# Kernel optimization log

Hardware: AMD Instinct MI355X
Metric: run time of the kernel (lower is better)

The kernel has to match this reference:

```python
import jax, jax.numpy as jnp
import numpy as np
import math

D = 128    # d_model
H = 8      # n_heads
NK = 16    # n_know
BS = 4
S = 256
DK = D // H
NEG = -1e32
LN_EPS = 1e-5


def _linear(x, W, b):
    return x @ W.T + b


def _layernorm(x, g, b):
    m = x.mean(-1, keepdims=True)
    v = ((x - m) ** 2).mean(-1, keepdims=True)
    return (x - m) / jnp.sqrt(v + LN_EPS) * g + b


def _attention(q, k, v, mask, gamma, maxout):
    # q,k,v: (B, H, S, DK); mask: (1,1,S,S) bool; gamma: (H,1,1)
    d_k = q.shape[-1]
    scores = jnp.einsum('bhid,bhjd->bhij', q, k) / math.sqrt(d_k)
    seqlen = scores.shape[-1]
    x = jnp.arange(seqlen, dtype=jnp.float32)
    pos = jnp.abs(x[None, :] - x[:, None])  # |j - i|, (S, S)
    # --- time-decay block (computed under no_grad in torch) ---
    s_ = jax.nn.softmax(jnp.where(mask, scores, NEG), axis=-1)
    distcum = jnp.cumsum(s_, axis=-1)
    disttotal = jnp.sum(s_, axis=-1, keepdims=True)
    dist = jnp.sqrt(jnp.clip((disttotal - distcum) * pos[None, None], 0.0, None))
    dist = jax.lax.stop_gradient(dist)
    effect = jnp.clip(jnp.exp(dist * (-jnp.abs(gamma)[None])), 1e-5, 1e5)
    scores = scores * effect
    scores = jax.nn.softmax(jnp.where(mask, scores, NEG), axis=-1)
    scores = jnp.where(mask, scores, 0.0)
    if maxout:
        scale = jnp.minimum(1.0 / scores.max(axis=-1, keepdims=True), 5.0)
        scores = scores * scale
    out = jnp.einsum('bhij,bhjd->bhid', scores, v)
    return out, scores


def _mha(q, k, v, mask, Wq, bq, Wk, bk, Wv, bv, Wo, bo, gamma, maxout):
    bs, seqlen, d = q.shape
    split = lambda x: x.reshape(bs, seqlen, H, DK).transpose(0, 2, 1, 3)
    qh = split(_linear(q, Wq, bq))
    kh = split(_linear(k, Wk, bk))
    vh = split(_linear(v, Wv, bv))
    out, scores = _attention(qh, kh, vh, mask, gamma, maxout)
    concat = out.transpose(0, 2, 1, 3).reshape(bs, seqlen, d)
    return _linear(concat, Wo, bo), scores


def _layer(query, key, values, peek_cur, Wq, bq, Wk, bk, Wv, bv, Wo, bo, gamma, lng, lnb):
    seqlen = query.shape[1]
    mask = jnp.tril(jnp.ones((seqlen, seqlen), bool), 0 if peek_cur else -1)[None, None]
    out, scores = _mha(query, key, values, mask, Wq, bq, Wk, bk, Wv, bv, Wo, bo, gamma,
                       maxout=not peek_cur)
    return _layernorm(query + out, lng, lnb), scores


def setup_inputs() -> dict:
    key = jax.random.key(0)
    ks = jax.random.split(key, 24)
    rn = lambda k, shape: (jax.random.normal(k, shape, jnp.float32) / math.sqrt(D))
    inp = {
        'q_emb': jax.random.normal(ks[0], (BS, S, D), jnp.float32),
        's_emb': jax.random.normal(ks[1], (BS, S, D), jnp.float32),
        'lens': jax.random.randint(ks[2], (BS,), 5, S),
        # block1 (kq_same=True -> shares Wq for K)
        'b1_Wq': rn(ks[3], (D, D)), 'b1_bq': jnp.zeros((D,), jnp.float32),
        'b1_Wv': rn(ks[4], (D, D)), 'b1_bv': jnp.zeros((D,), jnp.float32),
        'b1_Wo': rn(ks[5], (D, D)), 'b1_bo': jnp.zeros((D,), jnp.float32),
        'b1_gamma': jax.random.uniform(ks[6], (H, 1, 1), jnp.float32, -1.0, 1.0),
        'b1_lng': jnp.ones((D,), jnp.float32), 'b1_lnb': jnp.zeros((D,), jnp.float32),
        # block4 (kq_same=False)
        'b4_Wq': rn(ks[7], (D, D)), 'b4_bq': jnp.zeros((D,), jnp.float32),
        'b4_Wk': rn(ks[8], (D, D)), 'b4_bk': jnp.zeros((D,), jnp.float32),
        'b4_Wv': rn(ks[9], (D, D)), 'b4_bv': jnp.zeros((D,), jnp.float32),
        'b4_Wo': rn(ks[10], (D, D)), 'b4_bo': jnp.zeros((D,), jnp.float32),
        'b4_gamma': jax.random.uniform(ks[11], (H, 1, 1), jnp.float32, -1.0, 1.0),
        'b4_lng': jnp.ones((D,), jnp.float32), 'b4_lnb': jnp.zeros((D,), jnp.float32),
        'know_params': jax.random.uniform(ks[12], (NK, D), jnp.float32, -1.0, 1.0),
    }
    return inp


def reference(q_emb, s_emb, lens,
              b1_Wq, b1_bq, b1_Wv, b1_bv, b1_Wo, b1_bo, b1_gamma, b1_lng, b1_lnb,
              b4_Wq, b4_bq, b4_Wk, b4_bk, b4_Wv, b4_bv, b4_Wo, b4_bo, b4_gamma, b4_lng, b4_lnb,
              know_params):
    # n_layers == 1 path, eval mode (no mask dropout); lens unused in eval math.
    hq = q_emb
    p, q_scores = _layer(q_emb, q_emb, s_emb, True,
                         b1_Wq, b1_bq, b1_Wq, b1_bq, b1_Wv, b1_bv, b1_Wo, b1_bo,
                         b1_gamma, b1_lng, b1_lnb)
    bs, seqlen, d = p.shape
    query = jnp.broadcast_to(know_params[None, :, None, :], (bs, NK, seqlen, d)).reshape(bs * NK, seqlen, d)
    hq_r = jnp.broadcast_to(hq[:, None], (bs, NK, seqlen, d)).reshape(bs * NK, seqlen, d)
    p_r = jnp.broadcast_to(p[:, None], (bs, NK, seqlen, d)).reshape(bs * NK, seqlen, d)
    z, k_scores = _layer(query, hq_r, p_r, False,
                         b4_Wq, b4_bq, b4_Wk, b4_bk, b4_Wv, b4_bv, b4_Wo, b4_bo,
                         b4_gamma, b4_lng, b4_lnb)
    z = z.reshape(bs, NK, seqlen, d).transpose(0, 2, 1, 3).reshape(bs, seqlen, NK * d)
    k_scores = k_scores.reshape(bs, NK, H, seqlen, seqlen).transpose(0, 2, 3, 1, 4)
    return z, q_scores, k_scores
```

## Files before the change

### kernel.cpp

```cpp
#include <hip/hip_runtime.h>
#include <hip/hip_bf16.h>

#define DEV __device__ __forceinline__

DEV float4 f4fma(float4 a, float s, float4 w){
  a.x = fmaf(s, w.x, a.x); a.y = fmaf(s, w.y, a.y);
  a.z = fmaf(s, w.z, a.z); a.w = fmaf(s, w.w, a.w);
  return a;
}
DEV float4 f4add(float4 a, float4 b){
  a.x+=b.x; a.y+=b.y; a.z+=b.z; a.w+=b.w; return a;
}

DEV float waveAllMax(float x){
  #pragma unroll
  for(int o=1;o<64;o<<=1) x = fmaxf(x, __shfl_xor(x,o,64));
  return x;
}
DEV float waveAllSum(float x){
  #pragma unroll
  for(int o=1;o<64;o<<=1) x += __shfl_xor(x,o,64);
  return x;
}
DEV float waveReduceMax(float x){
  #pragma unroll
  for(int o=32;o>0;o>>=1) x = fmaxf(x, __shfl_down(x,o,64));
  return x;
}
DEV float blockMax256(float x, float* sc){
  int lane = threadIdx.x & 63, wid = threadIdx.x >> 6;
  x = waveReduceMax(x);
  __syncthreads();
  if(lane==0) sc[wid] = x;
  __syncthreads();
  return fmaxf(fmaxf(sc[0],sc[1]), fmaxf(sc[2],sc[3]));
}
DEV float blockScan256(float x, float* sc, float& total){
  int lane = threadIdx.x & 63, wid = threadIdx.x >> 6;
  float v = x;
  #pragma unroll
  for(int o=1;o<64;o<<=1){ float t = __shfl_up(v,o,64); if(lane>=o) v += t; }
  __syncthreads();
  if(lane==63) sc[wid] = v;
  __syncthreads();
  float pre=0.f, tot=0.f;
  #pragma unroll
  for(int ww=0;ww<4;ww++){ float s = sc[ww]; tot += s; if(ww<wid) pre += s; }
  total = tot;
  return v + pre;
}

template<int EPI>
DEV void gemm16_body(const float* __restrict__ in, const float* __restrict__ W,
                     const float* __restrict__ bias, const float* __restrict__ aux,
                     const float* __restrict__ lng, const float* __restrict__ lnb,
                     float* __restrict__ out, int r0, int nrows,
                     float* sWT, float (*sIn)[128])
{
  const int t = threadIdx.x;
  for(int idx=t; idx<2048; idx+=256){
    int r = idx>>7, c = idx&127;
    int row = r0+r;
    sIn[r][c] = (row<nrows) ? in[(size_t)row*128+c] : 0.f;
  }
  const int og = t & 31, rg = t >> 5;
  const int o0 = og*4;
  const float* s0p = sIn[rg*2];
  const float* s1p = sIn[rg*2+1];
  float4 a0 = make_float4(0,0,0,0), a1 = make_float4(0,0,0,0);

  #pragma unroll
  for(int half=0; half<2; half++){
    int c0 = half*64;
    __syncthreads();
    for(int idx=t; idx<8192; idx+=256){
      int o = idx>>6, cc = idx&63;
      sWT[cc*132 + o] = W[o*128 + c0 + cc];
    }
    __syncthreads();
    #pragma unroll 4
    for(int c=0;c<64;c+=4){
      float4 sA = *(const float4*)(s0p + c0 + c);
      float4 sB = *(const float4*)(s1p + c0 + c);
      const float* wp = sWT + c*132 + o0;
      float4 w0 = *(const float4*)(wp);
      float4 w1 = *(const float4*)(wp + 132);
      float4 w2 = *(const float4*)(wp + 264);
      float4 w3 = *(const float4*)(wp + 396);
      a0 = f4fma(a0, sA.x, w0); a0 = f4fma(a0, sA.y, w1);
      a0 = f4fma(a0, sA.z, w2); a0 = f4fma(a0, sA.w, w3);
      a1 = f4fma(a1, sB.x, w0); a1 = f4fma(a1, sB.y, w1);
      a1 = f4fma(a1, sB.z, w2); a1 = f4fma(a1, sB.w, w3);
    }
  }
  float4 bv = *(const float4*)(bias + o0);
  a0 = f4add(a0, bv); a1 = f4add(a1, bv);
  int row0 = r0 + rg*2, row1 = row0 + 1;

  if(EPI == 0){
    if(row0 < nrows) *(float4*)(out + (size_t)row0*128 + o0) = a0;
    if(row1 < nrows) *(float4*)(out + (size_t)row1*128 + o0) = a1;
  } else {
    const float *x0, *x1;
    if(EPI == 1){
      x0 = aux + (size_t)row0*128; x1 = aux + (size_t)row1*128;
    } else {
      x0 = aux + ((row0>>8)&15)*128; x1 = aux + ((row1>>8)&15)*128;
    }
    a0 = f4add(a0, *(const float4*)(x0 + o0));
    a1 = f4add(a1, *(const float4*)(x1 + o0));
    float s0 = a0.x+a0.y+a0.z+a0.w, s1 = a1.x+a1.y+a1.z+a1.w;
    float q0 = a0.x*a0.x+a0.y*a0.y+a0.z*a0.z+a0.w*a0.w;
    float q1 = a1.x*a1.x+a1.y*a1.y+a1.z*a1.z+a1.w*a1.w;
    #pragma unroll
    for(int o=1;o<32;o<<=1){
      s0 += __shfl_xor(s0,o,64); q0 += __shfl_xor(q0,o,64);
      s1 += __shfl_xor(s1,o,64); q1 += __shfl_xor(q1,o,64);
    }
    float m0 = s0*0.0078125f, v0 = q0*0.0078125f - m0*m0;
    float m1 = s1*0.0078125f, v1 = q1*0.0078125f - m1*m1;
    float i0 = rsqrtf(v0+1e-5f), i1 = rsqrtf(v1+1e-5f);
    float4 g  = *(const float4*)(lng + o0);
    float4 b2 = *(const float4*)(lnb + o0);
    float4 y0, y1;
    y0.x=(a0.x-m0)*i0*g.x+b2.x; y0.y=(a0.y-m0)*i0*g.y+b2.y;
    y0.z=(a0.z-m0)*i0*g.z+b2.z; y0.w=(a0.w-m0)*i0*g.w+b2.w;
    y1.x=(a1.x-m1)*i1*g.x+b2.x; y1.y=(a1.y-m1)*i1*g.y+b2.y;
    y1.z=(a1.z-m1)*i1*g.z+b2.z; y1.w=(a1.w-m1)*i1*g.w+b2.w;
    float *p0, *p1;
    if(EPI == 1){
      p0 = out + (size_t)row0*128; p1 = out + (size_t)row1*128;
    } else {
      int n0=(row0>>8)&15, b0=row0>>12, i0i=row0&255;
      int n1=(row1>>8)&15, b1=row1>>12, i1i=row1&255;
      p0 = out + ((((size_t)b0*256+i0i)*16+n0)<<7);
      p1 = out + ((((size_t)b1*256+i1i)*16+n1)<<7);
    }
    *(float4*)(p0 + o0) = y0;
    *(float4*)(p1 + o0) = y1;
  }
}

template<int EPI>
__global__ __launch_bounds__(256) void gemm16_kernel(
  const float* __restrict__ in, const float* __restrict__ W,
  const float* __restrict__ bias, const float* __restrict__ aux,
  const float* __restrict__ lng, const float* __restrict__ lnb,
  float* __restrict__ out, int nrows)
{
  __shared__ float sWT[64*132];
  __shared__ float sIn[16][128];
  gemm16_body<EPI>(in, W, bias, aux, lng, lnb, out, blockIdx.x*16, nrows, sWT, sIn);
}

__global__ __launch_bounds__(256) void proj4_kernel(
  const float* __restrict__ in0, const float* __restrict__ W0, const float* __restrict__ b0, float* __restrict__ o0,
  const float* __restrict__ in1, const float* __restrict__ W1, const float* __restrict__ b1, float* __restrict__ o1,
  const float* __restrict__ in2, const float* __restrict__ W2, const float* __restrict__ b2, float* __restrict__ o2,
  const float* __restrict__ in3, const float* __restrict__ W3, const float* __restrict__ b3, float* __restrict__ o3)
{
  __shared__ float sWT[64*132];
  __shared__ float sIn[16][128];
  int bb = blockIdx.x;
  if(bb < 64)       gemm16_body<0>(in0,W0,b0,nullptr,nullptr,nullptr,o0, bb*16,      1024, sWT,sIn);
  else if(bb < 128) gemm16_body<0>(in1,W1,b1,nullptr,nullptr,nullptr,o1,(bb-64)*16,  1024, sWT,sIn);
  else if(bb < 192) gemm16_body<0>(in2,W2,b2,nullptr,nullptr,nullptr,o2,(bb-128)*16, 1024, sWT,sIn);
  else              gemm16_body<0>(in3,W3,b3,nullptr,nullptr,nullptr,o3, 0,          16,   sWT,sIn);
}

__global__ __launch_bounds__(256) void attn1_kernel(
  const float* __restrict__ qk, const float* __restrict__ v1,
  const float* __restrict__ gamma, float* __restrict__ qs, float* __restrict__ aout)
{
  __shared__ float psW[4][256];
  int tile = blockIdx.x & 15;
  int bh   = blockIdx.x >> 4;
  int b = bh >> 3, h = bh & 7;
  int t = threadIdx.x, lane = t & 63, w = t >> 6;
  int d = lane & 15, jg = lane >> 4;
  int j0 = 4*lane;

  float4 kreg[4][4];
  #pragma unroll
  for(int u=0;u<4;u++){
    const float4* kr = (const float4*)(qk + (b*256 + j0 + u)*128 + h*16);
    kreg[u][0]=kr[0]; kreg[u][1]=kr[1]; kreg[u][2]=kr[2]; kreg[u][3]=kr[3];
  }
  float vreg[64];
  const float* vbase = v1 + (b*256 + jg*64)*128 + h*16 + d;
  #pragma unroll
  for(int k=0;k<64;k++) vreg[k] = vbase[k*128];

  float ga = fabsf(gamma[h]);

  for(int r=0;r<4;r++){
    int i = tile*16 + w*4 + r;
    const float4* qr = (const float4*)(qk + (b*256 + i)*128 + h*16);
    float4 q0=qr[0], q1=qr[1], q2=qr[2], q3=qr[3];

    float raw[4]; float mloc = -3e38f;
    #pragma unroll
    for(int u=0;u<4;u++){
      const float4* kk = kreg[u];
      float s = q0.x*kk[0].x + q0.y*kk[0].y + q0.z*kk[0].z + q0.w*kk[0].w
              + q1.x*kk[1].x + q1.y*kk[1].y + q1.z*kk[1].z + q1.w*kk[1].w
              + q2.x*kk[2].x + q2.y*kk[2].y + q2.z*kk[2].z + q2.w*kk[2].w
              + q3.x*kk[3].x + q3.y*kk[3].y + q3.z*kk[3].z + q3.w*kk[3].w;
      raw[u] = s * 0.25f;
      if(j0+u <= i) mloc = fmaxf(mloc, raw[u]);
    }
    float m1 = waveAllMax(mloc);
    float e[4], c[4]; float lsum = 0.f;
    #pragma unroll
    for(int u=0;u<4;u++){
      e[u] = (j0+u <= i) ? __expf(raw[u]-m1) : 0.f;
      lsum += e[u]; c[u] = lsum;
    }
    float s = lsum;
    #pragma unroll
    for(int o=1;o<64;o<<=1){ float tv = __shfl_up(s,o,64); if(lane>=o) s += tv; }
    float pre = s - lsum;
    float tot = __shfl(s, 63, 64);
    float invtot = 1.f/tot;

    float s2v[4]; float m2loc = -3e38f;
    #pragma unroll
    for(int u=0;u<4;u++){
      int j = j0+u;
      float cum  = (pre + c[u]) * invtot;
      float remn = fmaxf(1.f - cum, 0.f);
      float dist = sqrtf(remn * fabsf((float)(j - i)));
      float eff  = fminf(fmaxf(__expf(-ga*dist), 1e-5f), 1e5f);
      s2v[u] = raw[u]*eff;
      if(j <= i) m2loc = fmaxf(m2loc, s2v[u]);
    }
    float m2 = waveAllMax(m2loc);
    float e2[4]; float zloc = 0.f;
    #pragma unroll
    for(int u=0;u<4;u++){
      e2[u] = (j0+u <= i) ? __expf(s2v[u]-m2) : 0.f;
      zloc += e2[u];
    }
    float Z = waveAllSum(zloc);
    float invZ = 1.f/Z;
    float p0=e2[0]*invZ, p1=e2[1]*invZ, p2=e2[2]*invZ, p3=e2[3]*invZ;

    *(float4*)(qs + ((size_t)(bh*256 + i))*256 + j0) = make_float4(p0,p1,p2,p3);

    __syncthreads();
    *(float4*)&psW[w][j0] = make_float4(p0,p1,p2,p3);
    __syncthreads();
    float acc = 0.f;
    const float4* pw = (const float4*)&psW[w][jg*64];
    #pragma unroll
    for(int k=0;k<16;k++){
      float4 pk = pw[k];
      acc += pk.x*vreg[4*k] + pk.y*vreg[4*k+1] + pk.z*vreg[4*k+2] + pk.w*vreg[4*k+3];
    }
    acc += __shfl_xor(acc,16,64);
    acc += __shfl_xor(acc,32,64);
    if(lane < 16)
      aout[(b*256 + i)*128 + h*16 + d] = acc;
  }
}

DEV float dot16(const float* a, const float* b){
  float s = 0.f;
  #pragma unroll
  for(int k=0;k<16;k++) s += a[k]*b[k];
  return s;
}

__global__ __launch_bounds__(256) void attn4_pre(
  const float* __restrict__ q4, const float* __restrict__ k4,
  float* __restrict__ raw4, float* __restrict__ P4)
{
  __shared__ float sc4[4];
  int bnh = blockIdx.x;
  int b = bnh >> 7, n = (bnh >> 3) & 15, h = bnh & 7;
  int j = threadIdx.x;
  const float* qrow = q4 + n*128 + h*16;
  const float* krow = k4 + (b*256 + j)*128 + h*16;
  float raw = dot16(qrow, krow) * 0.25f;
  float M = blockMax256(raw, sc4);
  float E = __expf(raw - M);
  float tot;
  float P = blockScan256(E, sc4, tot);
  raw4[bnh*256 + j] = raw;
  P4[bnh*256 + j]   = P;
}

__global__ __launch_bounds__(256) void attn4_main(
  const float* __restrict__ raw4, const float* __restrict__ P4,
  const float* __restrict__ v4, const float* __restrict__ gamma,
  float* __restrict__ ks, float* __restrict__ aout)
{
  __shared__ float psW[4][256];
  int half = blockIdx.x & 1;
  int bnh  = blockIdx.x >> 1;
  int b = bnh >> 7, n = (bnh >> 3) & 15, h = bnh & 7;
  int t = threadIdx.x, lane = t & 63, w = t >> 6;
  int d = lane & 15, jg = lane >> 4;
  int j0 = 4*lane;

  float4 rw = *(const float4*)(raw4 + bnh*256 + j0);
  float4 Pv = *(const float4*)(P4   + bnh*256 + j0);
  const float* Pbase = P4 + bnh*256;

  float vreg[64];
  const float* vbase = v4 + (b*256 + jg*64)*128 + h*16 + d;
  #pragma unroll
  for(int k=0;k<64;k++) vreg[k] = vbase[k*128];

  float g4a = fabsf(gamma[h]);
  size_t ksrowbase = ((size_t)(b*8 + h)*256)*4096 + (size_t)n*256 + j0;
  float P_[4] = {Pv.x, Pv.y, Pv.z, Pv.w};
  float R_[4] = {rw.x, rw.y, rw.z, rw.w};

  for(int r=0;r<32;r++){
    int i = half*128 + w*32 + r;
    float p0=0.f,p1=0.f,p2=0.f,p3=0.f;
    if(i > 0){
      float invPm1 = 1.f / Pbase[i-1];
      float s2v[4]; float mloc = -3e38f;
      #pragma unroll
      for(int u=0;u<4;u++){
        int j = j0+u;
        float cum  = P_[u]*invPm1;
        float remn = fmaxf(1.f - cum, 0.f);
        float dist = sqrtf(remn * fabsf((float)(j - i)));
        float eff  = fminf(fmaxf(__expf(-g4a*dist), 1e-5f), 1e5f);
        float s2   = R_[u]*eff;
        s2v[u] = s2;
        if(j < i) mloc = fmaxf(mloc, s2);
      }
      float m2 = waveAllMax(mloc);
      float e_[4]; float zloc = 0.f;
      #pragma unroll
      for(int u=0;u<4;u++){
        float e = (j0+u < i) ? __expf(s2v[u]-m2) : 0.f;
        e_[u] = e; zloc += e;
      }
      float Z = waveAllSum(zloc);
      float sc = fminf(Z, 5.f)/Z;
      p0=e_[0]*sc; p1=e_[1]*sc; p2=e_[2]*sc; p3=e_[3]*sc;
    }
    *(float4*)(ks + ksrowbase + (size_t)i*4096) = make_float4(p0,p1,p2,p3);

    __syncthreads();
    *(float4*)&psW[w][j0] = make_float4(p0,p1,p2,p3);
    __syncthreads();
    float acc = 0.f;
    const float4* pw = (const float4*)&psW[w][jg*64];
    #pragma unroll
    for(int k=0;k<16;k++){
      float4 pk = pw[k];
      acc += pk.x*vreg[4*k] + pk.y*vreg[4*k+1] + pk.z*vreg[4*k+2] + pk.w*vreg[4*k+3];
    }
    acc += __shfl_xor(acc,16,64);
    acc += __shfl_xor(acc,32,64);
    if(lane < 16)
      aout[((b*16+n)*256 + i)*128 + h*16 + d] = acc;
  }
}

extern "C" void kernel_launch(void* const* d_in, const int* in_sizes, int n_in,
                              void* d_out, int out_size, void* d_ws, size_t ws_size,
                              hipStream_t stream)
{
  (void)in_sizes; (void)n_in; (void)out_size; (void)ws_size;
  const float* q_emb   = (const float*)d_in[0];
  const float* s_emb   = (const float*)d_in[1];
  const float* b1_Wq   = (const float*)d_in[3];
  const float* b1_bq   = (const float*)d_in[4];
  const float* b1_Wv   = (const float*)d_in[5];
  const float* b1_bv   = (const float*)d_in[6];
  const float* b1_Wo   = (const float*)d_in[7];
  const float* b1_bo   = (const float*)d_in[8];
  const float* b1_gamma= (const float*)d_in[9];
  const float* b1_lng  = (const float*)d_in[10];
  const float* b1_lnb  = (const float*)d_in[11];
  const float* b4_Wq   = (const float*)d_in[12];
  const float* b4_bq   = (const float*)d_in[13];
  const float* b4_Wk   = (const float*)d_in[14];
  const float* b4_bk   = (const float*)d_in[15];
  const float* b4_Wv   = (const float*)d_in[16];
  const float* b4_bv   = (const float*)d_in[17];
  const float* b4_Wo   = (const float*)d_in[18];
  const float* b4_bo   = (const float*)d_in[19];
  const float* b4_gamma= (const float*)d_in[20];
  const float* b4_lng  = (const float*)d_in[21];
  const float* b4_lnb  = (const float*)d_in[22];
  const float* know    = (const float*)d_in[23];

  float* w    = (float*)d_ws;
  float* qk1  = w;
  float* v1   = w + 131072;
  float* a1o  = w + 262144;
  float* p    = w + 393216;
  float* q4   = w + 524288;
  float* k4   = w + 526336;
  float* v4   = w + 657408;
  float* raw4 = w + 788480;
  float* P4   = w + 919552;
  float* a4o  = w + 1050624;

  float* z_out  = (float*)d_out;
  float* qs_out = z_out + 2097152;
  float* ks_out = z_out + 4194304;

  proj4_kernel<<<193,256,0,stream>>>(
      q_emb, b1_Wq, b1_bq, qk1,
      s_emb, b1_Wv, b1_bv, v1,
      q_emb, b4_Wk, b4_bk, k4,
      know,  b4_Wq, b4_bq, q4);

  attn1_kernel<<<512,256,0,stream>>>(qk1, v1, b1_gamma, qs_out, a1o);
  gemm16_kernel<1><<<64,256,0,stream>>>(a1o, b1_Wo, b1_bo, q_emb, b1_lng, b1_lnb, p, 1024);

  gemm16_kernel<0><<<64,256,0,stream>>>(p, b4_Wv, b4_bv, nullptr, nullptr, nullptr, v4, 1024);

  attn4_pre<<<512,256,0,stream>>>(q4, k4, raw4, P4);
  attn4_main<<<1024,256,0,stream>>>(raw4, P4, v4, b4_gamma, ks_out, a4o);

  gemm16_kernel<2><<<1024,256,0,stream>>>(a4o, b4_Wo, b4_bo, know, b4_lng, b4_lnb, z_out, 16384);
}
```

Baseline: 319.2 us.

## Fuse output projection with value projection and fold pre-pass into attention

Merges the layer-1 output projection plus layernorm and the layer-4 value projection into one kernel that reuses the normalized rows from shared memory. It also folds the attn4_pre score/scan pass into attn4_main, so each block recomputes the raw scores and prefix sums locally in shared memory instead of going through global scratch buffers. Together these remove two kernel launches and the global round trips for p, raw4 and P4. The cost is that the dot product and block scan are now computed twice, once by each of the two half-blocks per (b,n,h).

```diff
diff --git a/kernel.cpp b/kernel.cpp
--- a/kernel.cpp
+++ b/kernel.cpp
@@ -101,12 +101,8 @@
     if(row0 < nrows) *(float4*)(out + (size_t)row0*128 + o0) = a0;
     if(row1 < nrows) *(float4*)(out + (size_t)row1*128 + o0) = a1;
   } else {
-    const float *x0, *x1;
-    if(EPI == 1){
-      x0 = aux + (size_t)row0*128; x1 = aux + (size_t)row1*128;
-    } else {
-      x0 = aux + ((row0>>8)&15)*128; x1 = aux + ((row1>>8)&15)*128;
-    }
+    const float* x0 = aux + ((row0>>8)&15)*128;
+    const float* x1 = aux + ((row1>>8)&15)*128;
     a0 = f4add(a0, *(const float4*)(x0 + o0));
     a1 = f4add(a1, *(const float4*)(x1 + o0));
     float s0 = a0.x+a0.y+a0.z+a0.w, s1 = a1.x+a1.y+a1.z+a1.w;
@@ -127,15 +123,10 @@
     y0.z=(a0.z-m0)*i0*g.z+b2.z; y0.w=(a0.w-m0)*i0*g.w+b2.w;
     y1.x=(a1.x-m1)*i1*g.x+b2.x; y1.y=(a1.y-m1)*i1*g.y+b2.y;
     y1.z=(a1.z-m1)*i1*g.z+b2.z; y1.w=(a1.w-m1)*i1*g.w+b2.w;
-    float *p0, *p1;
-    if(EPI == 1){
-      p0 = out + (size_t)row0*128; p1 = out + (size_t)row1*128;
-    } else {
-      int n0=(row0>>8)&15, b0=row0>>12, i0i=row0&255;
-      int n1=(row1>>8)&15, b1=row1>>12, i1i=row1&255;
-      p0 = out + ((((size_t)b0*256+i0i)*16+n0)<<7);
-      p1 = out + ((((size_t)b1*256+i1i)*16+n1)<<7);
-    }
+    int n0=(row0>>8)&15, b0=row0>>12, i0i=row0&255;
+    int n1=(row1>>8)&15, b1=row1>>12, i1i=row1&255;
+    float* p0 = out + ((((size_t)b0*256+i0i)*16+n0)<<7);
+    float* p1 = out + ((((size_t)b1*256+i1i)*16+n1)<<7);
     *(float4*)(p0 + o0) = y0;
     *(float4*)(p1 + o0) = y1;
   }
@@ -166,6 +157,112 @@
   else if(bb < 128) gemm16_body<0>(in1,W1,b1,nullptr,nullptr,nullptr,o1,(bb-64)*16,  1024, sWT,sIn);
   else if(bb < 192) gemm16_body<0>(in2,W2,b2,nullptr,nullptr,nullptr,o2,(bb-128)*16, 1024, sWT,sIn);
   else              gemm16_body<0>(in3,W3,b3,nullptr,nullptr,nullptr,o3, 0,          16,   sWT,sIn);
+}
+
+__global__ __launch_bounds__(256) void gemm_p_v4(
+  const float* __restrict__ in, const float* __restrict__ Wo, const float* __restrict__ bo,
+  const float* __restrict__ resid, const float* __restrict__ lng, const float* __restrict__ lnb,
+  float* __restrict__ pout,
+  const float* __restrict__ Wv, const float* __restrict__ bvv, float* __restrict__ v4out)
+{
+  __shared__ float sWT[64*132];
+  __shared__ float sIn[16][128];
+  const int t = threadIdx.x;
+  const int r0 = blockIdx.x*16;
+  for(int idx=t; idx<2048; idx+=256){
+    int r = idx>>7, c = idx&127;
+    sIn[r][c] = in[(size_t)(r0+r)*128+c];
+  }
+  const int og = t & 31, rg = t >> 5;
+  const int o0 = og*4;
+  const float* s0p = sIn[rg*2];
+  const float* s1p = sIn[rg*2+1];
+  float4 a0 = make_float4(0,0,0,0), a1 = make_float4(0,0,0,0);
+
+  #pragma unroll
+  for(int half=0; half<2; half++){
+    int c0 = half*64;
+    __syncthreads();
+    for(int idx=t; idx<8192; idx+=256){
+      int o = idx>>6, cc = idx&63;
+      sWT[cc*132 + o] = Wo[o*128 + c0 + cc];
+    }
+    __syncthreads();
+    #pragma unroll 4
+    for(int c=0;c<64;c+=4){
+      float4 sA = *(const float4*)(s0p + c0 + c);
+      float4 sB = *(const float4*)(s1p + c0 + c);
+      const float* wp = sWT + c*132 + o0;
+      float4 w0 = *(const float4*)(wp);
+      float4 w1 = *(const float4*)(wp + 132);
+      float4 w2 = *(const float4*)(wp + 264);
+      float4 w3 = *(const float4*)(wp + 396);
+      a0 = f4fma(a0, sA.x, w0); a0 = f4fma(a0, sA.y, w1);
+      a0 = f4fma(a0, sA.z, w2); a0 = f4fma(a0, sA.w, w3);
+      a1 = f4fma(a1, sB.x, w0); a1 = f4fma(a1, sB.y, w1);
+      a1 = f4fma(a1, sB.z, w2); a1 = f4fma(a1, sB.w, w3);
+    }
+  }
+  int row0 = r0 + rg*2, row1 = row0 + 1;
+  {
+    float4 bv = *(const float4*)(bo + o0);
+    a0 = f4add(a0, bv); a1 = f4add(a1, bv);
+    a0 = f4add(a0, *(const float4*)(resid + (size_t)row0*128 + o0));
+    a1 = f4add(a1, *(const float4*)(resid + (size_t)row1*128 + o0));
+    float s0 = a0.x+a0.y+a0.z+a0.w, s1 = a1.x+a1.y+a1.z+a1.w;
+    float q0 = a0.x*a0.x+a0.y*a0.y+a0.z*a0.z+a0.w*a0.w;
+    float q1 = a1.x*a1.x+a1.y*a1.y+a1.z*a1.z+a1.w*a1.w;
+    #pragma unroll
+    for(int o=1;o<32;o<<=1){
+      s0 += __shfl_xor(s0,o,64); q0 += __shfl_xor(q0,o,64);
+      s1 += __shfl_xor(s1,o,64); q1 += __shfl_xor(q1,o,64);
+    }
+    float m0 = s0*0.0078125f, v0 = q0*0.0078125f - m0*m0;
+    float m1 = s1*0.0078125f, v1 = q1*0.0078125f - m1*m1;
+    float i0 = rsqrtf(v0+1e-5f), i1 = rsqrtf(v1+1e-5f);
+    float4 g  = *(const float4*)(lng + o0);
+    float4 b2 = *(const float4*)(lnb + o0);
+    float4 y0, y1;
+    y0.x=(a0.x-m0)*i0*g.x+b2.x; y0.y=(a0.y-m0)*i0*g.y+b2.y;
+    y0.z=(a0.z-m0)*i0*g.z+b2.z; y0.w=(a0.w-m0)*i0*g.w+b2.w;
+    y1.x=(a1.x-m1)*i1*g.x+b2.x; y1.y=(a1.y-m1)*i1*g.y+b2.y;
+    y1.z=(a1.z-m1)*i1*g.z+b2.z; y1.w=(a1.w-m1)*i1*g.w+b2.w;
+    *(float4*)(pout + (size_t)row0*128 + o0) = y0;
+    *(float4*)(pout + (size_t)row1*128 + o0) = y1;
+    __syncthreads();
+    *(float4*)&sIn[rg*2  ][o0] = y0;
+    *(float4*)&sIn[rg*2+1][o0] = y1;
+  }
+
+  a0 = make_float4(0,0,0,0); a1 = make_float4(0,0,0,0);
+  #pragma unroll
+  for(int half=0; half<2; half++){
+    int c0 = half*64;
+    __syncthreads();
+    for(int idx=t; idx<8192; idx+=256){
+      int o = idx>>6, cc = idx&63;
+      sWT[cc*132 + o] = Wv[o*128 + c0 + cc];
+    }
+    __syncthreads();
+    #pragma unroll 4
+    for(int c=0;c<64;c+=4){
+      float4 sA = *(const float4*)(s0p + c0 + c);
+      float4 sB = *(const float4*)(s1p + c0 + c);
+      const float* wp = sWT + c*132 + o0;
+      float4 w0 = *(const float4*)(wp);
+      float4 w1 = *(const float4*)(wp + 132);
+      float4 w2 = *(const float4*)(wp + 264);
+      float4 w3 = *(const float4*)(wp + 396);
+      a0 = f4fma(a0, sA.x, w0); a0 = f4fma(a0, sA.y, w1);
+      a0 = f4fma(a0, sA.z, w2); a0 = f4fma(a0, sA.w, w3);
+      a1 = f4fma(a1, sB.x, w0); a1 = f4fma(a1, sB.y, w1);
+      a1 = f4fma(a1, sB.z, w2); a1 = f4fma(a1, sB.w, w3);
+    }
+  }
+  float4 bv2 = *(const float4*)(bvv + o0);
+  a0 = f4add(a0, bv2); a1 = f4add(a1, bv2);
+  *(float4*)(v4out + (size_t)row0*128 + o0) = a0;
+  *(float4*)(v4out + (size_t)row1*128 + o0) = a1;
 }
 
 __global__ __launch_bounds__(256) void attn1_kernel(
@@ -271,30 +368,14 @@
   return s;
 }
 
-__global__ __launch_bounds__(256) void attn4_pre(
+__global__ __launch_bounds__(256) void attn4_main(
   const float* __restrict__ q4, const float* __restrict__ k4,
-  float* __restrict__ raw4, float* __restrict__ P4)
-{
-  __shared__ float sc4[4];
-  int bnh = blockIdx.x;
-  int b = bnh >> 7, n = (bnh >> 3) & 15, h = bnh & 7;
-  int j = threadIdx.x;
-  const float* qrow = q4 + n*128 + h*16;
-  const float* krow = k4 + (b*256 + j)*128 + h*16;
-  float raw = dot16(qrow, krow) * 0.25f;
-  float M = blockMax256(raw, sc4);
-  float E = __expf(raw - M);
-  float tot;
-  float P = blockScan256(E, sc4, tot);
-  raw4[bnh*256 + j] = raw;
-  P4[bnh*256 + j]   = P;
-}
-
-__global__ __launch_bounds__(256) void attn4_main(
-  const float* __restrict__ raw4, const float* __restrict__ P4,
   const float* __restrict__ v4, const float* __restrict__ gamma,
   float* __restrict__ ks, float* __restrict__ aout)
 {
+  __shared__ float sc4[4];
+  __shared__ float rawL[256];
+  __shared__ float PL[256];
   __shared__ float psW[4][256];
   int half = blockIdx.x & 1;
   int bnh  = blockIdx.x >> 1;
@@ -303,25 +384,36 @@
   int d = lane & 15, jg = lane >> 4;
   int j0 = 4*lane;
 
-  float4 rw = *(const float4*)(raw4 + bnh*256 + j0);
-  float4 Pv = *(const float4*)(P4   + bnh*256 + j0);
-  const float* Pbase = P4 + bnh*256;
-
+  {
+    const float* qrow = q4 + n*128 + h*16;
+    const float* krow = k4 + (b*256 + t)*128 + h*16;
+    float raw = dot16(qrow, krow) * 0.25f;
+    float M = blockMax256(raw, sc4);
+    float E = __expf(raw - M);
+    float tot;
+    float P = blockScan256(E, sc4, tot);
+    rawL[t] = raw;
+    PL[t]   = P;
+  }
   float vreg[64];
   const float* vbase = v4 + (b*256 + jg*64)*128 + h*16 + d;
   #pragma unroll
   for(int k=0;k<64;k++) vreg[k] = vbase[k*128];
+  __syncthreads();
+
+  float4 rw = *(const float4*)(rawL + j0);
+  float4 Pv = *(const float4*)(PL + j0);
+  float P_[4] = {Pv.x, Pv.y, Pv.z, Pv.w};
+  float R_[4] = {rw.x, rw.y, rw.z, rw.w};
 
   float g4a = fabsf(gamma[h]);
   size_t ksrowbase = ((size_t)(b*8 + h)*256)*4096 + (size_t)n*256 + j0;
-  float P_[4] = {Pv.x, Pv.y, Pv.z, Pv.w};
-  float R_[4] = {rw.x, rw.y, rw.z, rw.w};
 
   for(int r=0;r<32;r++){
     int i = half*128 + w*32 + r;
     float p0=0.f,p1=0.f,p2=0.f,p3=0.f;
     if(i > 0){
-      float invPm1 = 1.f / Pbase[i-1];
+      float invPm1 = 1.f / PL[i-1];
       float s2v[4]; float mloc = -3e38f;
       #pragma unroll
       for(int u=0;u<4;u++){
@@ -401,9 +493,7 @@
   float* q4   = w + 524288;
   float* k4   = w + 526336;
   float* v4   = w + 657408;
-  float* raw4 = w + 788480;
-  float* P4   = w + 919552;
-  float* a4o  = w + 1050624;
+  float* a4o  = w + 788480;
 
   float* z_out  = (float*)d_out;
   float* qs_out = z_out + 2097152;
@@ -416,12 +506,11 @@
       know,  b4_Wq, b4_bq, q4);
 
   attn1_kernel<<<512,256,0,stream>>>(qk1, v1, b1_gamma, qs_out, a1o);
-  gemm16_kernel<1><<<64,256,0,stream>>>(a1o, b1_Wo, b1_bo, q_emb, b1_lng, b1_lnb, p, 1024);
-
-  gemm16_kernel<0><<<64,256,0,stream>>>(p, b4_Wv, b4_bv, nullptr, nullptr, nullptr, v4, 1024);
-
-  attn4_pre<<<512,256,0,stream>>>(q4, k4, raw4, P4);
-  attn4_main<<<1024,256,0,stream>>>(raw4, P4, v4, b4_gamma, ks_out, a4o);
+
+  gemm_p_v4<<<64,256,0,stream>>>(a1o, b1_Wo, b1_bo, q_emb, b1_lng, b1_lnb, p,
+                                 b4_Wv, b4_bv, v4);
+
+  attn4_main<<<1024,256,0,stream>>>(q4, k4, v4, b4_gamma, ks_out, a4o);
 
   gemm16_kernel<2><<<1024,256,0,stream>>>(a4o, b4_Wo, b4_bo, know, b4_lng, b4_lnb, z_out, 16384);
 }
```

Result: faster. 308.4 us (-3.4%).
